# Kernel tuning notes

Measured on AMD Instinct MI355X. Metric: run time of the kernel, lower is better.

Reference implementation:

```python
import jax, jax.numpy as jnp
import numpy as np

N_EMBD = 1024
HEAD_SIZE = N_EMBD  # source bug: Block passes n_embd as head_size
EPS = 1e-5

def layernorm(x, g, b):
    mu = jnp.mean(x, axis=-1, keepdims=True)
    var = jnp.var(x, axis=-1, keepdims=True)
    return (x - mu) * jax.lax.rsqrt(var + EPS) * g + b

def setup_inputs() -> dict:
    key = jax.random.key(0)
    ks = jax.random.split(key, 8)
    B, T, C = 4, 2048, N_EMBD
    s = lambda fan_in: 1.0 / np.sqrt(fan_in)
    return {
        "x": jax.random.normal(ks[0], (B, T, C), dtype=jnp.float32),
        "Wk": jax.random.uniform(ks[1], (C, HEAD_SIZE), jnp.float32, -s(C), s(C)),
        "Wq": jax.random.uniform(ks[2], (C, HEAD_SIZE), jnp.float32, -s(C), s(C)),
        "Wv": jax.random.uniform(ks[3], (C, HEAD_SIZE), jnp.float32, -s(C), s(C)),
        "W1": jax.random.uniform(ks[4], (C, 4 * C), jnp.float32, -s(C), s(C)),
        "b1": jnp.zeros((4 * C,), jnp.float32),
        "W2": jax.random.uniform(ks[5], (4 * C, C), jnp.float32, -s(4 * C), s(4 * C)),
        "b2": jnp.zeros((C,), jnp.float32),
        "g1": jnp.ones((C,), jnp.float32),
        "be1": jnp.zeros((C,), jnp.float32),
        "g2": jnp.ones((C,), jnp.float32),
        "be2": jnp.zeros((C,), jnp.float32),
    }

def reference(x, Wk, Wq, Wv, W1, b1, W2, b2, g1, be1, g2, be2):
    B, T, C = x.shape
    h = layernorm(x, g1, be1)
    q = h @ Wq              # [B,T,H]
    k = h @ Wk
    v = h @ Wv
    wei = jnp.einsum('bth,bsh->bts', q, k) / jnp.sqrt(jnp.float32(C))
    causal = jnp.tril(jnp.ones((T, T), dtype=bool))
    wei = jnp.where(causal, wei, -jnp.inf)
    wei = jax.nn.softmax(wei, axis=-1)
    sa = jnp.einsum('bts,bsh->bth', wei, v)
    x = x + sa
    h2 = layernorm(x, g2, be2)
    ff = jax.nn.relu(h2 @ W1 + b1) @ W2 + b2
    return x + ff
```

## Files before the change

kernel.cpp:

```cpp
#include <hip/hip_runtime.h>
#include <hip/hip_bf16.h>


typedef __bf16 bf16x8_t __attribute__((ext_vector_type(8)));
typedef float f32x4_t __attribute__((ext_vector_type(4)));

__device__ __forceinline__ unsigned short f2bf(float f) {
    unsigned int u = __float_as_uint(f);
    u += 0x7fffu + ((u >> 16) & 1u);
    return (unsigned short)(u >> 16);
}
__device__ __forceinline__ float bf2f(unsigned short u) {
    return __uint_as_float((unsigned int)u << 16);
}

__device__ __forceinline__ void gload16(const void* g, void* lds) {
    __builtin_amdgcn_global_load_lds(
        (const __attribute__((address_space(1))) unsigned int*)g,
        (__attribute__((address_space(3))) unsigned int*)lds, 16, 0, 0);
}

#define SB0() __builtin_amdgcn_sched_barrier(0)
#define BAR_LGKM() asm volatile("s_barrier\ns_waitcnt lgkmcnt(0)" ::: "memory")
#define BAR() asm volatile("s_barrier" ::: "memory")
#define VM4_BAR() asm volatile("s_waitcnt vmcnt(4)\ns_barrier" ::: "memory")
#define VM0_BAR() asm volatile("s_waitcnt vmcnt(0)\ns_barrier" ::: "memory")

enum { EPI_F32 = 0, EPI_BF16 = 1, EPI_BIAS_RELU_BF16 = 2, EPI_RESID_F32 = 3,
       EPI_BIAS_RESID_F32 = 4 };

template <int EPI, bool CSKIP, bool KLIM>
__global__ __launch_bounds__(512, 2) void gemm256(
    const unsigned short* __restrict__ A,
    const unsigned short* __restrict__ Bm,
    void* __restrict__ Cout,
    const float* __restrict__ bias,
    const float* __restrict__ resid,
    int M, int N, int K, int lda, int ldb, float scale,
    long long batA, long long batB, long long batC, long long batR)
{
    __shared__ __align__(16) unsigned char lds[131072];

    const int gx = gridDim.x;
    const int nwg = gx * gridDim.y;
    int bl = blockIdx.y * gx + blockIdx.x;
    bl = (bl & 7) * (nwg >> 3) + (bl >> 3);
    const int bx = bl % gx, by = bl / gx;

    const int row0 = by * 256, col0 = bx * 256;
    if (CSKIP && col0 > row0) return;

    const int bz = blockIdx.z;
    const unsigned short* Ab = A + (long long)bz * batA + (long long)row0 * lda;
    const unsigned short* Bb = Bm + (long long)bz * batB + (long long)col0 * ldb;

    const int tid = threadIdx.x, lane = tid & 63, wid = tid >> 6;
    const int wrM = (wid >> 2) * 128;
    const int wcN = (wid & 3) * 64;
    const int lr = lane & 15, lg = lane >> 4;

    int Keff = K;
    if (KLIM) { int kl = row0 + 256; Keff = kl < K ? kl : K; }
    const int nkt = Keff >> 6;

    const int c0 = wid * 128 + lane;
    const int crow = c0 >> 2;
    const int sg = (c0 & 3) ^ ((c0 >> 3) & 3);
    const unsigned short* gA0 = Ab + (long long)crow * lda + sg * 8;
    const unsigned short* gA1 = gA0 + 16ll * lda;
    const unsigned short* gB0 = Bb + (long long)crow * ldb + sg * 8;
    const unsigned short* gB1 = gB0 + 16ll * ldb;

    const int sw = (lg ^ ((lr >> 1) & 3)) << 4;
    const int aoff = (wrM + lr) * 64 + sw;
    const int boff = 16384 + (wcN + lr) * 64 + sw;

    f32x4_t acc[8][4];
#pragma unroll
    for (int m = 0; m < 8; ++m)
#pragma unroll
        for (int n = 0; n < 4; ++n)
            acc[m][n] = (f32x4_t){0.f, 0.f, 0.f, 0.f};

    auto stageR = [&](int b, int r, int ktn) {
        const int kk = r >> 1, op = r & 1;
        const int ke = ktn * 64 + kk * 32;
        unsigned char* d = lds + b * 65536 + kk * 32768 + op * 16384 + wid * 2048;
        const unsigned short* g0 = (op ? gB0 : gA0) + ke;
        const unsigned short* g1 = (op ? gB1 : gA1) + ke;
        gload16(g0, d);
        gload16(g1, d + 1024);
    };

    bf16x8_t af[4], bv[4];
    auto dsA4 = [&](int b, int kk, int mq) {
        const unsigned char* u = lds + b * 65536 + kk * 32768;
#pragma unroll
        for (int j = 0; j < 4; ++j)
            af[j] = *(const bf16x8_t*)(u + aoff + (mq * 4 + j) * 1024);
    };
    auto dsB4 = [&](int b, int kk) {
        const unsigned char* u = lds + b * 65536 + kk * 32768;
#pragma unroll
        for (int n = 0; n < 4; ++n)
            bv[n] = *(const bf16x8_t*)(u + boff + n * 1024);
    };
    auto mf16 = [&](int mq) {
        __builtin_amdgcn_s_setprio(1);
#pragma unroll
        for (int j = 0; j < 4; ++j)
#pragma unroll
            for (int n = 0; n < 4; ++n)
                acc[mq * 4 + j][n] = __builtin_amdgcn_mfma_f32_16x16x32_bf16(
                    af[j], bv[n], acc[mq * 4 + j][n], 0, 0, 0);
        __builtin_amdgcn_s_setprio(0);
    };

    stageR(0, 0, 0); stageR(0, 1, 0); stageR(0, 2, 0); stageR(0, 3, 0);
    VM4_BAR();

    int kt = 0;
    for (; kt < nkt - 1; ++kt) {
        const int buf = kt & 1, nb = buf ^ 1;
        dsA4(buf, 0, 0); dsB4(buf, 0);
        stageR(nb, 0, kt + 1);
        BAR_LGKM(); SB0();
        mf16(0); SB0();
        BAR();
        dsA4(buf, 0, 1);
        stageR(nb, 1, kt + 1);
        BAR_LGKM(); SB0();
        mf16(1); SB0();
        VM4_BAR();
        dsA4(buf, 1, 0); dsB4(buf, 1);
        stageR(nb, 2, kt + 1);
        BAR_LGKM(); SB0();
        mf16(0); SB0();
        BAR();
        dsA4(buf, 1, 1);
        stageR(nb, 3, kt + 1);
        BAR_LGKM(); SB0();
        mf16(1); SB0();
        VM4_BAR();
    }
    {
        const int buf = kt & 1;
        dsA4(buf, 0, 0); dsB4(buf, 0);
        BAR_LGKM(); SB0();
        mf16(0); SB0();
        BAR();
        dsA4(buf, 0, 1);
        BAR_LGKM(); SB0();
        mf16(1); SB0();
        VM0_BAR();
        dsA4(buf, 1, 0); dsB4(buf, 1);
        BAR_LGKM(); SB0();
        mf16(0); SB0();
        BAR();
        dsA4(buf, 1, 1);
        BAR_LGKM(); SB0();
        mf16(1); SB0();
    }

    const int ldc = N;
    float* Cf = (float*)Cout + (long long)bz * batC;
    unsigned short* Cb = (unsigned short*)Cout + (long long)bz * batC;
    const float* R = nullptr;
    if constexpr (EPI == EPI_RESID_F32 || EPI == EPI_BIAS_RESID_F32)
        R = resid + (long long)bz * batR;

#pragma unroll
    for (int m = 0; m < 8; ++m)
#pragma unroll
        for (int n = 0; n < 4; ++n)
#pragma unroll
            for (int j = 0; j < 4; ++j) {
                const int row = row0 + wrM + m * 16 + lg * 4 + j;
                const int col = col0 + wcN + n * 16 + lr;
                const long long idx = (long long)row * ldc + col;
                float v = acc[m][n][j] * scale;
                if constexpr (EPI == EPI_F32) {
                    Cf[idx] = v;
                } else if constexpr (EPI == EPI_BF16) {
                    Cb[idx] = f2bf(v);
                } else if constexpr (EPI == EPI_BIAS_RELU_BF16) {
                    v += bias[col];
                    v = v > 0.f ? v : 0.f;
                    Cb[idx] = f2bf(v);
                } else if constexpr (EPI == EPI_RESID_F32) {
                    Cf[idx] = v + R[idx];
                } else {
                    Cf[idx] = v + bias[col] + R[idx];
                }
            }
}

template <int EPI, bool CSKIP, bool KLIM>
__global__ __launch_bounds__(256, 2) void gemm128(
    const unsigned short* __restrict__ A,
    const unsigned short* __restrict__ Bm,
    void* __restrict__ Cout,
    const float* __restrict__ bias,
    const float* __restrict__ resid,
    int M, int N, int K, int lda, int ldb, float scale,
    long long batA, long long batB, long long batC, long long batR)
{
    __shared__ __align__(16) unsigned char lds[65536];

    const int gx = gridDim.x;
    const int nwg = gx * gridDim.y;
    int bl = blockIdx.y * gx + blockIdx.x;
    bl = (bl & 7) * (nwg >> 3) + (bl >> 3);
    const int bx = bl % gx, by = bl / gx;

    const int row0 = by * 128, col0 = bx * 128;
    if (CSKIP && col0 > row0) return;

    const int bz = blockIdx.z;
    const unsigned short* Ab = A + (long long)bz * batA + (long long)row0 * lda;
    const unsigned short* Bb = Bm + (long long)bz * batB + (long long)col0 * ldb;

    const int tid = threadIdx.x, lane = tid & 63, wid = tid >> 6;
    const int wrM = (wid >> 1) * 64;
    const int wcN = (wid & 1) * 64;
    const int lr = lane & 15, lg = lane >> 4;

    int Keff = K;
    if (KLIM) { int kl = row0 + 128; Keff = kl < K ? kl : K; }
    const int nkt = Keff >> 6;

    const int c0 = wid * 128 + lane;
    const int crow = c0 >> 2;
    const int sg = (c0 & 3) ^ ((c0 >> 3) & 3);
    const unsigned short* gA0 = Ab + (long long)crow * lda + sg * 8;
    const unsigned short* gA1 = gA0 + 16ll * lda;
    const unsigned short* gB0 = Bb + (long long)crow * ldb + sg * 8;
    const unsigned short* gB1 = gB0 + 16ll * ldb;

    const int sw = (lg ^ ((lr >> 1) & 3)) << 4;
    const int aoff = (wrM + lr) * 64 + sw;
    const int boff = 8192 + (wcN + lr) * 64 + sw;

    f32x4_t acc[4][4];
#pragma unroll
    for (int m = 0; m < 4; ++m)
#pragma unroll
        for (int n = 0; n < 4; ++n)
            acc[m][n] = (f32x4_t){0.f, 0.f, 0.f, 0.f};

    auto stage2 = [&](int b, int kk, int ktn) {
        const int ke = ktn * 64 + kk * 32;
        unsigned char* uA = lds + b * 32768 + kk * 16384 + wid * 2048;
        unsigned char* uB = uA + 8192;
        gload16(gA0 + ke, uA);
        gload16(gA1 + ke, uA + 1024);
        gload16(gB0 + ke, uB);
        gload16(gB1 + ke, uB + 1024);
    };

    bf16x8_t af[4], bv[4];
    auto dsAB = [&](int b, int kk) {
        const unsigned char* u = lds + b * 32768 + kk * 16384;
#pragma unroll
        for (int m = 0; m < 4; ++m)
            af[m] = *(const bf16x8_t*)(u + aoff + m * 1024);
#pragma unroll
        for (int n = 0; n < 4; ++n)
            bv[n] = *(const bf16x8_t*)(u + boff + n * 1024);
    };
    auto mf16 = [&]() {
        __builtin_amdgcn_s_setprio(1);
#pragma unroll
        for (int m = 0; m < 4; ++m)
#pragma unroll
            for (int n = 0; n < 4; ++n)
                acc[m][n] = __builtin_amdgcn_mfma_f32_16x16x32_bf16(
                    af[m], bv[n], acc[m][n], 0, 0, 0);
        __builtin_amdgcn_s_setprio(0);
    };

    stage2(0, 0, 0); stage2(0, 1, 0);
    VM4_BAR();

    int kt = 0;
    for (; kt < nkt - 1; ++kt) {
        const int buf = kt & 1, nb = buf ^ 1;
        dsAB(buf, 0);
        stage2(nb, 0, kt + 1);
        BAR_LGKM(); SB0();
        mf16(); SB0();
        VM4_BAR();
        dsAB(buf, 1);
        stage2(nb, 1, kt + 1);
        BAR_LGKM(); SB0();
        mf16(); SB0();
        VM4_BAR();
    }
    {
        const int buf = kt & 1;
        dsAB(buf, 0);
        BAR_LGKM(); SB0();
        mf16(); SB0();
        VM0_BAR();
        dsAB(buf, 1);
        BAR_LGKM(); SB0();
        mf16(); SB0();
    }

    const int ldc = N;
    float* Cf = (float*)Cout + (long long)bz * batC;
    unsigned short* Cb = (unsigned short*)Cout + (long long)bz * batC;
    const float* R = nullptr;
    if constexpr (EPI == EPI_RESID_F32 || EPI == EPI_BIAS_RESID_F32)
        R = resid + (long long)bz * batR;

#pragma unroll
    for (int m = 0; m < 4; ++m)
#pragma unroll
        for (int n = 0; n < 4; ++n)
#pragma unroll
            for (int j = 0; j < 4; ++j) {
                const int row = row0 + wrM + m * 16 + lg * 4 + j;
                const int col = col0 + wcN + n * 16 + lr;
                const long long idx = (long long)row * ldc + col;
                float v = acc[m][n][j] * scale;
                if constexpr (EPI == EPI_F32) {
                    Cf[idx] = v;
                } else if constexpr (EPI == EPI_BF16) {
                    Cb[idx] = f2bf(v);
                } else if constexpr (EPI == EPI_BIAS_RELU_BF16) {
                    v += bias[col];
                    v = v > 0.f ? v : 0.f;
                    Cb[idx] = f2bf(v);
                } else if constexpr (EPI == EPI_RESID_F32) {
                    Cf[idx] = v + R[idx];
                } else {
                    Cf[idx] = v + bias[col] + R[idx];
                }
            }
}

__global__ __launch_bounds__(256, 2) void pv_k(
    const unsigned short* __restrict__ Pm,
    const unsigned short* __restrict__ vT,
    float* __restrict__ xres,
    const float* __restrict__ x,
    int Tt, int Cc, int BT)
{
    __shared__ __align__(16) unsigned char lds[65536];

    const int gx = gridDim.x;
    const int nwg = gx * gridDim.y;
    int bl = blockIdx.y * gx + blockIdx.x;
    bl = (bl & 7) * (nwg >> 3) + (bl >> 3);
    const int bx = bl % gx, by = bl / gx;
    const int bz = blockIdx.z;

    const int col0 = bx * 128;
    const int tid = threadIdx.x, lane = tid & 63, wid = tid >> 6;
    const int wrM = (wid >> 1) * 64;
    const int wcN = (wid & 1) * 64;
    const int lr = lane & 15, lg = lane >> 4;

    const int c0 = wid * 128 + lane;
    const int crow = c0 >> 2;
    const int sg = (c0 & 3) ^ ((c0 >> 3) & 3);

    const int lda = Tt, ldb = BT, ldc = Cc;
    const unsigned short* Bb = vT + (long long)bz * Tt + (long long)col0 * ldb;
    const unsigned short* gB0 = Bb + (long long)crow * ldb + sg * 8;
    const unsigned short* gB1 = gB0 + 16ll * ldb;

    const int sw = (lg ^ ((lr >> 1) & 3)) << 4;
    const int aoff = (wrM + lr) * 64 + sw;
    const int boff = 8192 + (wcN + lr) * 64 + sw;

    bf16x8_t af[4], bv[4];
    auto dsAB = [&](int b, int kk) {
        const unsigned char* u = lds + b * 32768 + kk * 16384;
#pragma unroll
        for (int m = 0; m < 4; ++m)
            af[m] = *(const bf16x8_t*)(u + aoff + m * 1024);
#pragma unroll
        for (int n = 0; n < 4; ++n)
            bv[n] = *(const bf16x8_t*)(u + boff + n * 1024);
    };

    float* Cf = xres + (long long)bz * Tt * Cc;
    const float* R = x + (long long)bz * Tt * Cc;

    for (int pass = 0; pass < 2; ++pass) {
        const int by_eff = pass ? (15 - by) : by;
        const int row0 = by_eff * 128;
        const int nkt = (row0 + 128) >> 6;

        const unsigned short* Ab = Pm + (long long)bz * Tt * Tt + (long long)row0 * lda;
        const unsigned short* gA0 = Ab + (long long)crow * lda + sg * 8;
        const unsigned short* gA1 = gA0 + 16ll * lda;

        auto stage2 = [&](int b, int kk, int ktn) {
            const int ke = ktn * 64 + kk * 32;
            unsigned char* uA = lds + b * 32768 + kk * 16384 + wid * 2048;
            unsigned char* uB = uA + 8192;
            gload16(gA0 + ke, uA);
            gload16(gA1 + ke, uA + 1024);
            gload16(gB0 + ke, uB);
            gload16(gB1 + ke, uB + 1024);
        };

        f32x4_t acc[4][4];
#pragma unroll
        for (int m = 0; m < 4; ++m)
#pragma unroll
            for (int n = 0; n < 4; ++n)
                acc[m][n] = (f32x4_t){0.f, 0.f, 0.f, 0.f};

        auto mf16 = [&]() {
            __builtin_amdgcn_s_setprio(1);
#pragma unroll
            for (int m = 0; m < 4; ++m)
#pragma unroll
                for (int n = 0; n < 4; ++n)
                    acc[m][n] = __builtin_amdgcn_mfma_f32_16x16x32_bf16(
                        af[m], bv[n], acc[m][n], 0, 0, 0);
            __builtin_amdgcn_s_setprio(0);
        };

        if (pass) BAR();
        stage2(0, 0, 0); stage2(0, 1, 0);
        VM4_BAR();

        int kt = 0;
        for (; kt < nkt - 1; ++kt) {
            const int buf = kt & 1, nb = buf ^ 1;
            dsAB(buf, 0);
            stage2(nb, 0, kt + 1);
            BAR_LGKM(); SB0();
            mf16(); SB0();
            VM4_BAR();
            dsAB(buf, 1);
            stage2(nb, 1, kt + 1);
            BAR_LGKM(); SB0();
            mf16(); SB0();
            VM4_BAR();
        }
        {
            const int buf = kt & 1;
            dsAB(buf, 0);
            BAR_LGKM(); SB0();
            mf16(); SB0();
            VM0_BAR();
            dsAB(buf, 1);
            BAR_LGKM(); SB0();
            mf16(); SB0();
        }

#pragma unroll
        for (int m = 0; m < 4; ++m)
#pragma unroll
            for (int n = 0; n < 4; ++n)
#pragma unroll
                for (int j = 0; j < 4; ++j) {
                    const int row = row0 + wrM + m * 16 + lg * 4 + j;
                    const int col = col0 + wcN + n * 16 + lr;
                    const long long idx = (long long)row * ldc + col;
                    Cf[idx] = acc[m][n][j] + R[idx];
                }
    }
}

__global__ __launch_bounds__(256) void tconv_k(
    const float* __restrict__ in, unsigned short* __restrict__ out,
    int R, int Cc)
{
    __shared__ float t[64][65];
    const int r0 = blockIdx.y * 64, c0 = blockIdx.x * 64;
    const int tid = threadIdx.x;
    const int a = tid >> 4;
    const int b = tid & 15;
#pragma unroll
    for (int i = 0; i < 4; ++i) {
        const int row = a + i * 16;
        float4 v = *(const float4*)(in + (long long)(r0 + row) * Cc + c0 + b * 4);
        t[row][b * 4 + 0] = v.x; t[row][b * 4 + 1] = v.y;
        t[row][b * 4 + 2] = v.z; t[row][b * 4 + 3] = v.w;
    }
    __syncthreads();
#pragma unroll
    for (int i = 0; i < 4; ++i) {
        const int oc = a + i * 16;
        ushort4 o;
        o.x = f2bf(t[b * 4 + 0][oc]);
        o.y = f2bf(t[b * 4 + 1][oc]);
        o.z = f2bf(t[b * 4 + 2][oc]);
        o.w = f2bf(t[b * 4 + 3][oc]);
        *(ushort4*)(out + (long long)(c0 + oc) * R + r0 + b * 4) = o;
    }
}

__global__ __launch_bounds__(256) void vtrans_k(
    const unsigned short* __restrict__ in, unsigned short* __restrict__ out)
{
    __shared__ unsigned short t[64][72];
    const int r0 = blockIdx.x * 64;
    const int c0 = blockIdx.y * 64;
    const int tid = threadIdx.x;
#pragma unroll
    for (int i = 0; i < 2; ++i) {
        const int ch = tid * 2 + i;
        const int row = ch >> 3, cs = ch & 7;
        int4 v = *(const int4*)(in + (long long)(r0 + row) * 3072 + 2048 + c0 + cs * 8);
        *(int4*)&t[row][cs * 8] = v;
    }
    __syncthreads();
#pragma unroll
    for (int i = 0; i < 2; ++i) {
        const int w = tid * 2 + i;
        const int oc = w >> 3, orc = w & 7;
        unsigned short tmp[8];
#pragma unroll
        for (int j = 0; j < 8; ++j) tmp[j] = t[orc * 8 + j][oc];
        *(int4*)(out + (long long)(c0 + oc) * 8192 + r0 + orc * 8) = *(const int4*)tmp;
    }
}

__global__ __launch_bounds__(256) void ln_k(
    const float* __restrict__ x, const float* __restrict__ g,
    const float* __restrict__ be, unsigned short* __restrict__ out)
{
    const int wv = threadIdx.x >> 6, lane = threadIdx.x & 63;
    const long long row = blockIdx.x * 4 + wv;
    const float* xr = x + row * 1024;
    float4 v[4];
    float s = 0.f, q = 0.f;
#pragma unroll
    for (int j = 0; j < 4; ++j) {
        v[j] = *(const float4*)(xr + j * 256 + lane * 4);
        s += v[j].x + v[j].y + v[j].z + v[j].w;
        q += v[j].x * v[j].x + v[j].y * v[j].y + v[j].z * v[j].z + v[j].w * v[j].w;
    }
#pragma unroll
    for (int off = 32; off > 0; off >>= 1) {
        s += __shfl_xor(s, off);
        q += __shfl_xor(q, off);
    }
    const float mean = s * (1.0f / 1024.0f);
    const float var  = q * (1.0f / 1024.0f) - mean * mean;
    const float rstd = rsqrtf(var + 1e-5f);
#pragma unroll
    for (int j = 0; j < 4; ++j) {
        float4 gv = *(const float4*)(g + j * 256 + lane * 4);
        float4 bv = *(const float4*)(be + j * 256 + lane * 4);
        ushort4 o;
        o.x = f2bf((v[j].x - mean) * rstd * gv.x + bv.x);
        o.y = f2bf((v[j].y - mean) * rstd * gv.y + bv.y);
        o.z = f2bf((v[j].z - mean) * rstd * gv.z + bv.z);
        o.w = f2bf((v[j].w - mean) * rstd * gv.w + bv.w);
        *(ushort4*)(out + row * 1024 + j * 256 + lane * 4) = o;
    }
}

__global__ __launch_bounds__(256) void softmax_k(
    const unsigned short* __restrict__ S, unsigned short* __restrict__ P, int T)
{
    const int wv = threadIdx.x >> 6, lane = threadIdx.x & 63;
    const int t = blockIdx.x * 4 + wv;
    const long long base = ((long long)blockIdx.y * T + t) * (long long)T;
    const unsigned short* srow = S + base;
    unsigned short* prow = P + base;
    const int n = t + 1;
    const int lim = ((t >> 7) + 1) << 7;
    const int nch = (lim + 511) >> 9;

    float v[4][8];
    float mx = -3.0e38f;
#pragma unroll
    for (int j = 0; j < 4; ++j) {
        if (j < nch) {
            const int e0 = (j * 64 + lane) * 8;
            int4 r = *(const int4*)(srow + e0);
            const unsigned short* u = (const unsigned short*)&r;
#pragma unroll
            for (int i = 0; i < 8; ++i) {
                float f = bf2f(u[i]);
                v[j][i] = f;
                if (e0 + i < n) mx = fmaxf(mx, f);
            }
        }
    }
#pragma unroll
    for (int off = 32; off > 0; off >>= 1) mx = fmaxf(mx, __shfl_xor(mx, off));

    float sum = 0.f;
#pragma unroll
    for (int j = 0; j < 4; ++j) {
        if (j < nch) {
            const int e0 = (j * 64 + lane) * 8;
#pragma unroll
            for (int i = 0; i < 8; ++i) {
                float e = (e0 + i < n) ? __expf(v[j][i] - mx) : 0.f;
                v[j][i] = e;
                sum += e;
            }
        }
    }
#pragma unroll
    for (int off = 32; off > 0; off >>= 1) sum += __shfl_xor(sum, off);
    const float inv = 1.0f / sum;

#pragma unroll
    for (int j = 0; j < 4; ++j) {
        if (j < nch) {
            const int e0 = (j * 64 + lane) * 8;
            unsigned short o[8];
#pragma unroll
            for (int i = 0; i < 8; ++i) o[i] = f2bf(v[j][i] * inv);
            *(int4*)(prow + e0) = *(const int4*)o;
        }
    }
}

extern "C" void kernel_launch(void* const* d_in, const int* in_sizes, int n_in,
                              void* d_out, int out_size, void* d_ws, size_t ws_size,
                              hipStream_t stream)
{
    const int B = 4, T = 2048, C = 1024, F = 4096;
    const float* x   = (const float*)d_in[0];
    const float* Wk  = (const float*)d_in[1];
    const float* Wq  = (const float*)d_in[2];
    const float* Wv  = (const float*)d_in[3];
    const float* W1  = (const float*)d_in[4];
    const float* b1  = (const float*)d_in[5];
    const float* W2  = (const float*)d_in[6];
    const float* b2  = (const float*)d_in[7];
    const float* g1  = (const float*)d_in[8];
    const float* be1 = (const float*)d_in[9];
    const float* g2  = (const float*)d_in[10];
    const float* be2 = (const float*)d_in[11];

    char* ws = (char*)d_ws;
    const size_t MB = 1ull << 20;
    unsigned short* h     = (unsigned short*)(ws + 0);
    unsigned short* qkv   = (unsigned short*)(ws + 16 * MB);
    unsigned short* vT    = (unsigned short*)(ws + 64 * MB);
    float*          xres  = (float*)(ws + 80 * MB);
    unsigned short* S     = (unsigned short*)(ws + 112 * MB);
    unsigned short* P     = (unsigned short*)(ws + 144 * MB);
    unsigned short* ff1   = (unsigned short*)(ws + 112 * MB);
    unsigned short* wqkvT = (unsigned short*)(ws + 176 * MB);
    unsigned short* w1T   = (unsigned short*)(ws + 182 * MB);
    unsigned short* w2T   = (unsigned short*)(ws + 190 * MB);

    tconv_k<<<dim3(16, 16), 256, 0, stream>>>(Wq, wqkvT, C, C);
    tconv_k<<<dim3(16, 16), 256, 0, stream>>>(Wk, wqkvT + C * C, C, C);
    tconv_k<<<dim3(16, 16), 256, 0, stream>>>(Wv, wqkvT + 2 * C * C, C, C);
    tconv_k<<<dim3(64, 16), 256, 0, stream>>>(W1, w1T, C, F);
    tconv_k<<<dim3(16, 64), 256, 0, stream>>>(W2, w2T, F, C);

    ln_k<<<dim3(B * T / 4), 256, 0, stream>>>(x, g1, be1, h);

    dim3 gqkv(3 * C / 256, (B * T) / 256, 1);
    gemm256<EPI_BF16, false, false><<<gqkv, 512, 0, stream>>>(
        h, wqkvT, qkv, nullptr, nullptr, B * T, 3 * C, C, C, C, 1.0f, 0, 0, 0, 0);

    vtrans_k<<<dim3(B * T / 64, C / 64), 256, 0, stream>>>(qkv, vT);

    dim3 gsc(T / 256, T / 256, B);
    gemm256<EPI_BF16, true, false><<<gsc, 512, 0, stream>>>(
        qkv, qkv + C, S, nullptr, nullptr, T, T, C, 3 * C, 3 * C, 0.03125f,
        (long long)T * 3 * C, (long long)T * 3 * C, (long long)T * T, 0);

    softmax_k<<<dim3(T / 4, B), 256, 0, stream>>>(S, P, T);

    pv_k<<<dim3(C / 128, 8, B), 256, 0, stream>>>(
        P, vT, xres, x, T, C, B * T);

    ln_k<<<dim3(B * T / 4), 256, 0, stream>>>(xres, g2, be2, h);

    dim3 gf1(F / 256, (B * T) / 256, 1);
    gemm256<EPI_BIAS_RELU_BF16, false, false><<<gf1, 512, 0, stream>>>(
        h, w1T, ff1, b1, nullptr, B * T, F, C, C, C, 1.0f, 0, 0, 0, 0);

    dim3 gf2(C / 128, (B * T) / 128, 1);
    gemm128<EPI_BIAS_RESID_F32, false, false><<<gf2, 256, 0, stream>>>(
        ff1, w2T, (float*)d_out, b2, xres, B * T, C, F, F, F, 1.0f, 0, 0, 0, 0);
}
```

Baseline: 358.1 us.

## Compute V transposed directly and fuse it with causal score GEMM launch

The QKV projection is split: Q and K are produced by the existing GEMM, while V is computed already transposed (Wv^T · h^T) in a new kernel. That kernel shares a grid with the causal QK^T score GEMM, so the blocks left idle by skipped upper-triangle tiles compute V^T tiles instead. This removes the separate vtrans kernel and the extra write and read of V, and fills the idle causal blocks. It costs a dedicated 128KB-LDS kernel with a remapped block index, and the mapping of idle blocks to V tiles must cover exactly 128 tiles.

```diff
diff --git a/kernel.cpp b/kernel.cpp
--- a/kernel.cpp
+++ b/kernel.cpp
@@ -192,6 +192,165 @@
                 } else {
                     Cf[idx] = v + bias[col] + R[idx];
                 }
+            }
+}
+
+__global__ __launch_bounds__(512, 2) void sc_vt_k(
+    const unsigned short* __restrict__ qk,
+    const unsigned short* __restrict__ wvT,
+    const unsigned short* __restrict__ h,
+    unsigned short* __restrict__ Sm,
+    unsigned short* __restrict__ vTo)
+{
+    __shared__ __align__(16) unsigned char lds[131072];
+
+    int bl = blockIdx.y * 8 + blockIdx.x;
+    bl = (bl & 7) * 9 + (bl >> 3);
+    const int bx = bl & 7, by = bl >> 3;
+    const int z = blockIdx.z;
+
+    const unsigned short* Ab;
+    const unsigned short* Bb;
+    unsigned short* Cb;
+    int lda, ldb, ldc, row0, col0;
+    float scale;
+
+    if (by < 8 && bx <= by) {
+        row0 = by * 256; col0 = bx * 256;
+        lda = 2048; ldb = 2048; ldc = 2048;
+        Ab = qk + ((long long)z * 2048 + row0) * 2048;
+        Bb = qk + ((long long)z * 2048 + col0) * 2048 + 1024;
+        Cb = Sm + (long long)z * 2048 * 2048;
+        scale = 0.03125f;
+    } else {
+        int d;
+        if (by < 8) d = z * 28 + ((bx * (bx - 1)) >> 1) + by;
+        else        d = 112 + z * 8 + bx;
+        if (d >= 128) return;
+        const int rt = d >> 5, ct = d & 31;
+        row0 = rt * 256; col0 = ct * 256;
+        lda = 1024; ldb = 1024; ldc = 8192;
+        Ab = wvT + (long long)row0 * 1024;
+        Bb = h + (long long)col0 * 1024;
+        Cb = vTo;
+        scale = 1.0f;
+    }
+    Ab += 0; Bb += 0;
+
+    const int tid = threadIdx.x, lane = tid & 63, wid = tid >> 6;
+    const int wrM = (wid >> 2) * 128;
+    const int wcN = (wid & 3) * 64;
+    const int lr = lane & 15, lg = lane >> 4;
+    const int nkt = 16;
+
+    const int c0 = wid * 128 + lane;
+    const int crow = c0 >> 2;
+    const int sg = (c0 & 3) ^ ((c0 >> 3) & 3);
+    const unsigned short* gA0 = Ab + (long long)crow * lda + sg * 8;
+    const unsigned short* gA1 = gA0 + 16ll * lda;
+    const unsigned short* gB0 = Bb + (long long)crow * ldb + sg * 8;
+    const unsigned short* gB1 = gB0 + 16ll * ldb;
+
+    const int sw = (lg ^ ((lr >> 1) & 3)) << 4;
+    const int aoff = (wrM + lr) * 64 + sw;
+    const int boff = 16384 + (wcN + lr) * 64 + sw;
+
+    f32x4_t acc[8][4];
+#pragma unroll
+    for (int m = 0; m < 8; ++m)
+#pragma unroll
+        for (int n = 0; n < 4; ++n)
+            acc[m][n] = (f32x4_t){0.f, 0.f, 0.f, 0.f};
+
+    auto stageR = [&](int b, int r, int ktn) {
+        const int kk = r >> 1, op = r & 1;
+        const int ke = ktn * 64 + kk * 32;
+        unsigned char* d = lds + b * 65536 + kk * 32768 + op * 16384 + wid * 2048;
+        const unsigned short* g0 = (op ? gB0 : gA0) + ke;
+        const unsigned short* g1 = (op ? gB1 : gA1) + ke;
+        gload16(g0, d);
+        gload16(g1, d + 1024);
+    };
+
+    bf16x8_t af[4], bv[4];
+    auto dsA4 = [&](int b, int kk, int mq) {
+        const unsigned char* u = lds + b * 65536 + kk * 32768;
+#pragma unroll
+        for (int j = 0; j < 4; ++j)
+            af[j] = *(const bf16x8_t*)(u + aoff + (mq * 4 + j) * 1024);
+    };
+    auto dsB4 = [&](int b, int kk) {
+        const unsigned char* u = lds + b * 65536 + kk * 32768;
+#pragma unroll
+        for (int n = 0; n < 4; ++n)
+            bv[n] = *(const bf16x8_t*)(u + boff + n * 1024);
+    };
+    auto mf16 = [&](int mq) {
+        __builtin_amdgcn_s_setprio(1);
+#pragma unroll
+        for (int j = 0; j < 4; ++j)
+#pragma unroll
+            for (int n = 0; n < 4; ++n)
+                acc[mq * 4 + j][n] = __builtin_amdgcn_mfma_f32_16x16x32_bf16(
+                    af[j], bv[n], acc[mq * 4 + j][n], 0, 0, 0);
+        __builtin_amdgcn_s_setprio(0);
+    };
+
+    stageR(0, 0, 0); stageR(0, 1, 0); stageR(0, 2, 0); stageR(0, 3, 0);
+    VM4_BAR();
+
+    int kt = 0;
+    for (; kt < nkt - 1; ++kt) {
+        const int buf = kt & 1, nb = buf ^ 1;
+        dsA4(buf, 0, 0); dsB4(buf, 0);
+        stageR(nb, 0, kt + 1);
+        BAR_LGKM(); SB0();
+        mf16(0); SB0();
+        BAR();
+        dsA4(buf, 0, 1);
+        stageR(nb, 1, kt + 1);
+        BAR_LGKM(); SB0();
+        mf16(1); SB0();
+        VM4_BAR();
+        dsA4(buf, 1, 0); dsB4(buf, 1);
+        stageR(nb, 2, kt + 1);
+        BAR_LGKM(); SB0();
+        mf16(0); SB0();
+        BAR();
+        dsA4(buf, 1, 1);
+        stageR(nb, 3, kt + 1);
+        BAR_LGKM(); SB0();
+        mf16(1); SB0();
+        VM4_BAR();
+    }
+    {
+        const int buf = kt & 1;
+        dsA4(buf, 0, 0); dsB4(buf, 0);
+        BAR_LGKM(); SB0();
+        mf16(0); SB0();
+        BAR();
+        dsA4(buf, 0, 1);
+        BAR_LGKM(); SB0();
+        mf16(1); SB0();
+        VM0_BAR();
+        dsA4(buf, 1, 0); dsB4(buf, 1);
+        BAR_LGKM(); SB0();
+        mf16(0); SB0();
+        BAR();
+        dsA4(buf, 1, 1);
+        BAR_LGKM(); SB0();
+        mf16(1); SB0();
+    }
+
+#pragma unroll
+    for (int m = 0; m < 8; ++m)
+#pragma unroll
+        for (int n = 0; n < 4; ++n)
+#pragma unroll
+            for (int j = 0; j < 4; ++j) {
+                const int row = row0 + wrM + m * 16 + lg * 4 + j;
+                const int col = col0 + wcN + n * 16 + lr;
+                Cb[(long long)row * ldc + col] = f2bf(acc[m][n][j] * scale);
             }
 }
 
@@ -498,32 +657,6 @@
     }
 }
 
-__global__ __launch_bounds__(256) void vtrans_k(
-    const unsigned short* __restrict__ in, unsigned short* __restrict__ out)
-{
-    __shared__ unsigned short t[64][72];
-    const int r0 = blockIdx.x * 64;
-    const int c0 = blockIdx.y * 64;
-    const int tid = threadIdx.x;
-#pragma unroll
-    for (int i = 0; i < 2; ++i) {
-        const int ch = tid * 2 + i;
-        const int row = ch >> 3, cs = ch & 7;
-        int4 v = *(const int4*)(in + (long long)(r0 + row) * 3072 + 2048 + c0 + cs * 8);
-        *(int4*)&t[row][cs * 8] = v;
-    }
-    __syncthreads();
-#pragma unroll
-    for (int i = 0; i < 2; ++i) {
-        const int w = tid * 2 + i;
-        const int oc = w >> 3, orc = w & 7;
-        unsigned short tmp[8];
-#pragma unroll
-        for (int j = 0; j < 8; ++j) tmp[j] = t[orc * 8 + j][oc];
-        *(int4*)(out + (long long)(c0 + oc) * 8192 + r0 + orc * 8) = *(const int4*)tmp;
-    }
-}
-
 __global__ __launch_bounds__(256) void ln_k(
     const float* __restrict__ x, const float* __restrict__ g,
     const float* __restrict__ be, unsigned short* __restrict__ out)
@@ -640,35 +773,31 @@
 
     char* ws = (char*)d_ws;
     const size_t MB = 1ull << 20;
-    unsigned short* h     = (unsigned short*)(ws + 0);
-    unsigned short* qkv   = (unsigned short*)(ws + 16 * MB);
-    unsigned short* vT    = (unsigned short*)(ws + 64 * MB);
-    float*          xres  = (float*)(ws + 80 * MB);
-    unsigned short* S     = (unsigned short*)(ws + 112 * MB);
-    unsigned short* P     = (unsigned short*)(ws + 144 * MB);
-    unsigned short* ff1   = (unsigned short*)(ws + 112 * MB);
-    unsigned short* wqkvT = (unsigned short*)(ws + 176 * MB);
-    unsigned short* w1T   = (unsigned short*)(ws + 182 * MB);
-    unsigned short* w2T   = (unsigned short*)(ws + 190 * MB);
-
-    tconv_k<<<dim3(16, 16), 256, 0, stream>>>(Wq, wqkvT, C, C);
-    tconv_k<<<dim3(16, 16), 256, 0, stream>>>(Wk, wqkvT + C * C, C, C);
-    tconv_k<<<dim3(16, 16), 256, 0, stream>>>(Wv, wqkvT + 2 * C * C, C, C);
+    unsigned short* h    = (unsigned short*)(ws + 0);
+    unsigned short* qk   = (unsigned short*)(ws + 16 * MB);
+    unsigned short* vT   = (unsigned short*)(ws + 64 * MB);
+    float*          xres = (float*)(ws + 80 * MB);
+    unsigned short* S    = (unsigned short*)(ws + 112 * MB);
+    unsigned short* P    = (unsigned short*)(ws + 144 * MB);
+    unsigned short* ff1  = (unsigned short*)(ws + 112 * MB);
+    unsigned short* wqkT = (unsigned short*)(ws + 176 * MB);
+    unsigned short* wvT  = (unsigned short*)(ws + 180 * MB);
+    unsigned short* w1T  = (unsigned short*)(ws + 182 * MB);
+    unsigned short* w2T  = (unsigned short*)(ws + 190 * MB);
+
+    tconv_k<<<dim3(16, 16), 256, 0, stream>>>(Wq, wqkT, C, C);
+    tconv_k<<<dim3(16, 16), 256, 0, stream>>>(Wk, wqkT + C * C, C, C);
+    tconv_k<<<dim3(16, 16), 256, 0, stream>>>(Wv, wvT, C, C);
     tconv_k<<<dim3(64, 16), 256, 0, stream>>>(W1, w1T, C, F);
     tconv_k<<<dim3(16, 64), 256, 0, stream>>>(W2, w2T, F, C);
 
     ln_k<<<dim3(B * T / 4), 256, 0, stream>>>(x, g1, be1, h);
 
-    dim3 gqkv(3 * C / 256, (B * T) / 256, 1);
-    gemm256<EPI_BF16, false, false><<<gqkv, 512, 0, stream>>>(
-        h, wqkvT, qkv, nullptr, nullptr, B * T, 3 * C, C, C, C, 1.0f, 0, 0, 0, 0);
-
-    vtrans_k<<<dim3(B * T / 64, C / 64), 256, 0, stream>>>(qkv, vT);
-
-    dim3 gsc(T / 256, T / 256, B);
-    gemm256<EPI_BF16, true, false><<<gsc, 512, 0, stream>>>(
-        qkv, qkv + C, S, nullptr, nullptr, T, T, C, 3 * C, 3 * C, 0.03125f,
-        (long long)T * 3 * C, (long long)T * 3 * C, (long long)T * T, 0);
+    dim3 gqk(2 * C / 256, (B * T) / 256, 1);
+    gemm256<EPI_BF16, false, false><<<gqk, 512, 0, stream>>>(
+        h, wqkT, qk, nullptr, nullptr, B * T, 2 * C, C, C, C, 1.0f, 0, 0, 0, 0);
+
+    sc_vt_k<<<dim3(8, 9, B), 512, 0, stream>>>(qk, wvT, h, S, vT);
 
     softmax_k<<<dim3(T / 4, B), 256, 0, stream>>>(S, P, T);
 
```

New measurement: 343.6 us. -4.0%, faster.
